# Performance work log

Measured on AMD Instinct MI355X. Metric: run time of the kernel, lower is better.

Reference implementation:

```python
import jax, jax.numpy as jnp
import numpy as np

B, N, DIM, NL, E = 8, 4096, 128, 3, 524288
NN = B * N


def setup_inputs() -> dict:
    key = jax.random.key(0)
    kx, ke, kw = jax.random.split(key, 3)
    x = jax.random.normal(kx, (B, N, DIM), dtype=jnp.float32)
    batch_edge_index = jax.random.randint(ke, (2, E), 0, NN, dtype=jnp.int32)
    wks = jax.random.split(kw, NL)
    Ws = jnp.stack([jax.random.normal(k, (DIM, DIM), dtype=jnp.float32) / np.sqrt(DIM)
                    for k in wks])  # [NL, DIM, DIM]
    bs = jnp.zeros((NL, DIM), dtype=jnp.float32)
    return {"x": x, "batch_edge_index": batch_edge_index, "Ws": Ws, "bs": bs}


def _gcn_layer(x, W, b, row, col, deg_inv_sqrt, n):
    # PyG GCNConv: h = x @ W; symmetric normalization over edges+self-loops;
    # scatter-add messages at targets (col); add bias.
    h = x @ W  # [n, DIM]
    norm = deg_inv_sqrt[row] * deg_inv_sqrt[col]  # [E+n]
    msg = h[row] * norm[:, None]  # gather at sources, scale
    return jax.ops.segment_sum(msg, col, num_segments=n) + b


def reference(x, batch_edge_index, Ws, bs):
    nb, npts, d = x.shape
    n = nb * npts
    h = x.reshape(n, d)
    # add self-loops once (same edge structure for all layers)
    loops = jnp.arange(n, dtype=batch_edge_index.dtype)
    row = jnp.concatenate([batch_edge_index[0], loops])
    col = jnp.concatenate([batch_edge_index[1], loops])
    deg = jax.ops.segment_sum(jnp.ones_like(col, dtype=h.dtype), col, num_segments=n)
    deg_inv_sqrt = jnp.where(deg > 0, jax.lax.rsqrt(jnp.maximum(deg, 1e-12)), 0.0)
    for i in range(NL):
        out = _gcn_layer(h, Ws[i], bs[i], row, col, deg_inv_sqrt, n)
        h = jax.nn.relu(h + out)  # residual + relu (dropout = identity in eval)
    return h.reshape(nb, npts, d)
```

## Files before the change

### kernel.cpp

```cpp
#include <hip/hip_runtime.h>


typedef __attribute__((ext_vector_type(8))) short short8;
typedef __attribute__((ext_vector_type(4))) float f32x4;
typedef __attribute__((ext_vector_type(2))) float f32x2;
typedef __attribute__((ext_vector_type(2))) unsigned u32x2;

__device__ inline ushort f2bf(float f) {
    union { float f; unsigned u; } v; v.f = f;
    unsigned u = v.u;
    return (ushort)((u + 0x7fffu + ((u >> 16) & 1u)) >> 16);
}
__device__ inline float2 bf2f(unsigned u) {
    union { unsigned i; float f; } a, b;
    a.i = u << 16;
    b.i = u & 0xffff0000u;
    return make_float2(a.f, b.f);
}
__device__ inline f32x4 bf4(u32x2 v) {
    float2 a = bf2f(v.x), b = bf2f(v.y);
    f32x4 r = { a.x, a.y, b.x, b.y };
    return r;
}
__device__ inline short8 pack8(f32x4 a, f32x4 b) {
    short8 r = { (short)f2bf(a.x), (short)f2bf(a.y), (short)f2bf(a.z), (short)f2bf(a.w),
                 (short)f2bf(b.x), (short)f2bf(b.y), (short)f2bf(b.z), (short)f2bf(b.w) };
    return r;
}
__device__ inline unsigned char f2fp8(float f) {
    return (unsigned char)(__builtin_amdgcn_cvt_pk_fp8_f32(f, f, 0, false) & 0xff);
}
__device__ inline unsigned pack4fp8(f32x4 v) {
    unsigned u = (unsigned)__builtin_amdgcn_cvt_pk_fp8_f32(v.x, v.y, 0, false);
    u = (unsigned)__builtin_amdgcn_cvt_pk_fp8_f32(v.z, v.w, (int)u, true);
    return u;
}
__device__ inline f32x4 fp8x4(unsigned v) {
    f32x2 lo = __builtin_amdgcn_cvt_pk_f32_fp8((int)v, false);
    f32x2 hi = __builtin_amdgcn_cvt_pk_f32_fp8((int)v, true);
    f32x4 r = { lo.x, lo.y, hi.x, hi.y };
    return r;
}

__global__ __launch_bounds__(256) void k_scan1(const int* __restrict__ deg,
                                               int* __restrict__ offs,
                                               int* __restrict__ bsum, int n) {
    __shared__ int sm[256];
    int t = threadIdx.x, i = blockIdx.x * 256 + t;
    int v = (i < n) ? deg[i] : 0;
    sm[t] = v;
    __syncthreads();
    for (int off = 1; off < 256; off <<= 1) {
        int u = (t >= off) ? sm[t - off] : 0;
        __syncthreads();
        sm[t] += u;
        __syncthreads();
    }
    if (i < n) offs[i] = sm[t] - v;
    if (t == 255) bsum[blockIdx.x] = sm[255];
}

__global__ __launch_bounds__(256) void k_scan3(int* __restrict__ offs,
                                               const int* __restrict__ bsum,
                                               const int* __restrict__ deg,
                                               int* __restrict__ cnt,
                                               float* __restrict__ dis,
                                               unsigned* __restrict__ g32,
                                               int n, int E) {
    __shared__ int red[256];
    int t = threadIdx.x, bid = blockIdx.x;
    red[t] = (t < 128 && t < bid) ? bsum[t] : 0;
    __syncthreads();
    for (int off = 128; off >= 1; off >>= 1) {
        if (t < off) red[t] += red[t + off];
        __syncthreads();
    }
    int base = red[0];
    int i = bid * 256 + t;
    float dv = 0.f;
    if (i < n) {
        int o = offs[i] + base;
        offs[i] = o;
        cnt[i] = o;
        dv = rsqrtf((float)(deg[i] + 1));
        dis[i] = dv;
    }
    if (i == 0) offs[n] = E;
    if (i < 32) g32[(size_t)n * 32 + i] = 0;

    int lane = t & 63;
    int wbase = bid * 256 + (t & ~63);
    int hl = lane & 31, sel = lane >> 5;
    for (int rr = 0; rr < 64; rr += 2) {
        int row = wbase + rr + sel;
        float d = __shfl(dv, rr + sel, 64);
        if (row < n) {
            unsigned u = g32[(size_t)row * 32 + hl];
            g32[(size_t)row * 32 + hl] = pack4fp8(fp8x4(u) * d);
        }
    }
}

__global__ void k_csr(const int* __restrict__ row, const int* __restrict__ col,
                      int* __restrict__ cnt, ushort* __restrict__ csru, int E) {
    int i = blockIdx.x * blockDim.x + threadIdx.x;
    if (i < E) {
        int c = col[i];
        int p = atomicAdd(&cnt[c], 1);
        csru[p] = (ushort)row[i];
    }
}

#define GEMM_MAIN(A0, A1, A2, A3)                                               \
    f32x4 acc[8] = {};                                                          \
    _Pragma("unroll")                                                           \
    for (int nf = 0; nf < 8; ++nf) {                                            \
        const unsigned* wr = &Wl[nf * 16 + c][0];                               \
        int sx = (c & 7) << 2;                                                  \
        int b = q * 4;                                                          \
        short8 b0 = *(const short8*)(wr + ((b +  0) ^ sx));                     \
        short8 b1 = *(const short8*)(wr + ((b + 16) ^ sx));                     \
        short8 b2 = *(const short8*)(wr + ((b + 32) ^ sx));                     \
        short8 b3 = *(const short8*)(wr + ((b + 48) ^ sx));                     \
        acc[nf] = __builtin_amdgcn_mfma_f32_16x16x32_bf16(A0, b0, acc[nf], 0, 0, 0); \
        acc[nf] = __builtin_amdgcn_mfma_f32_16x16x32_bf16(A1, b1, acc[nf], 0, 0, 0); \
        acc[nf] = __builtin_amdgcn_mfma_f32_16x16x32_bf16(A2, b2, acc[nf], 0, 0, 0); \
        acc[nf] = __builtin_amdgcn_mfma_f32_16x16x32_bf16(A3, b3, acc[nf], 0, 0, 0); \
    }

#define GEMM_STORE(D0, D1, D2, D3)                                              \
    _Pragma("unroll")                                                           \
    for (int nf = 0; nf < 8; ++nf) {                                            \
        int gc = nf * 16 + c;                                                   \
        g[(size_t)(rb + q * 4 + 0) * 128 + gc] = f2fp8(acc[nf][0] * (D0));      \
        g[(size_t)(rb + q * 4 + 1) * 128 + gc] = f2fp8(acc[nf][1] * (D1));      \
        g[(size_t)(rb + q * 4 + 2) * 128 + gc] = f2fp8(acc[nf][2] * (D2));      \
        g[(size_t)(rb + q * 4 + 3) * 128 + gc] = f2fp8(acc[nf][3] * (D3));      \
    }

#define W_STAGE(TILE)                                                            \
    __shared__ unsigned Wl[128][64];                                             \
    int tid = threadIdx.x;                                                       \
    {                                                                            \
        int nn = tid & 127, hf = tid >> 7;                                       \
        for (int qq = 0; qq < 32; ++qq) {                                        \
            int k2 = hf * 32 + qq;                                               \
            float lo = W[(size_t)(2 * k2) * 128 + nn];                           \
            float hi = W[(size_t)(2 * k2 + 1) * 128 + nn];                       \
            Wl[nn][k2 ^ ((nn & 7) << 2)] = ((unsigned)f2bf(hi) << 16) | f2bf(lo);\
        }                                                                        \
    }                                                                            \
    __syncthreads();                                                             \
    int w = tid >> 6, l = tid & 63;                                              \
    int rb = (TILE) * 64 + w * 16;                                               \
    int c = l & 15, q = l >> 4;

__global__ __launch_bounds__(256) void k_gemm(const unsigned* __restrict__ hb,
                                              const float* __restrict__ W,
                                              const float* __restrict__ dis,
                                              unsigned char* __restrict__ g, int n) {
    W_STAGE(blockIdx.x)
    const short8* arow = (const short8*)(hb + (size_t)(rb + c) * 64);
    short8 a0 = arow[q], a1 = arow[4 + q], a2 = arow[8 + q], a3 = arow[12 + q];
    GEMM_MAIN(a0, a1, a2, a3)
    float d0 = dis[rb + q * 4 + 0], d1 = dis[rb + q * 4 + 1];
    float d2 = dis[rb + q * 4 + 2], d3 = dis[rb + q * 4 + 3];
    GEMM_STORE(d0, d1, d2, d3)
}

__global__ __launch_bounds__(256) void k_l0(const float* __restrict__ x,
                                            const float* __restrict__ W,
                                            unsigned char* __restrict__ g,
                                            const int* __restrict__ col,
                                            int* __restrict__ deg,
                                            int n, int E) {
    int gtiles = n >> 6;
    if ((int)blockIdx.x >= gtiles) {
        int i = ((int)blockIdx.x - gtiles) * 256 + threadIdx.x;
        if (i < E) atomicAdd(&deg[col[i]], 1);
        return;
    }
    W_STAGE((int)blockIdx.x)
    const f32x4* xr = (const f32x4*)(x + (size_t)(rb + c) * 128);
    short8 a0 = pack8(xr[q * 2 +  0], xr[q * 2 +  1]);
    short8 a1 = pack8(xr[q * 2 +  8], xr[q * 2 +  9]);
    short8 a2 = pack8(xr[q * 2 + 16], xr[q * 2 + 17]);
    short8 a3 = pack8(xr[q * 2 + 24], xr[q * 2 + 25]);
    GEMM_MAIN(a0, a1, a2, a3)
    GEMM_STORE(1.f, 1.f, 1.f, 1.f)
}

__global__ __launch_bounds__(256) void k_gather(const unsigned* __restrict__ g32,
                                                unsigned* __restrict__ hb,
                                                const float* __restrict__ dis,
                                                const float* __restrict__ bias,
                                                const int* __restrict__ offs,
                                                const ushort* __restrict__ csru,
                                                const float* __restrict__ xres,
                                                float* __restrict__ outp,
                                                int n, int use_x, int last) {
    int wid = threadIdx.x >> 6, lane = threadIdx.x & 63;
    int sel = lane >> 5, hl = lane & 31;
    int node = blockIdx.x * 8 + wid * 2 + sel;
    if (node >= n) return;

    f32x4 acc = fp8x4(g32[(size_t)node * 32 + hl]);
    int s = offs[node];
    int deg = offs[node + 1] - s;
    for (int j0 = 0; j0 < deg; j0 += 32) {
        int rem = deg - j0;
        int m = rem < 32 ? rem : 32;
        int idx = (hl < m) ? (int)__builtin_nontemporal_load(&csru[s + j0 + hl]) : n;
        int mc = (m + 15) & ~15;
        for (int t = 0; t < mc; t += 16) {
            unsigned v[16];
#pragma unroll
            for (int u = 0; u < 16; ++u) {
                int r = __shfl(idx, t + u, 32);
                v[u] = g32[(size_t)r * 32 + hl];
            }
            f32x4 s0 = (fp8x4(v[0]) + fp8x4(v[1])) + (fp8x4(v[2]) + fp8x4(v[3]));
            f32x4 s1 = (fp8x4(v[4]) + fp8x4(v[5])) + (fp8x4(v[6]) + fp8x4(v[7]));
            f32x4 s2 = (fp8x4(v[8]) + fp8x4(v[9])) + (fp8x4(v[10]) + fp8x4(v[11]));
            f32x4 s3 = (fp8x4(v[12]) + fp8x4(v[13])) + (fp8x4(v[14]) + fp8x4(v[15]));
            acc += (s0 + s1) + (s2 + s3);
        }
    }
    float dn = dis[node];
    f32x4 bv = ((const f32x4*)bias)[hl];
    f32x4 hv;
    if (use_x) {
        hv = __builtin_nontemporal_load(&((const f32x4*)xres)[(size_t)node * 32 + hl]);
    } else {
        u32x2 h2 = __builtin_nontemporal_load(&((const u32x2*)hb)[(size_t)node * 32 + hl]);
        hv = bf4(h2);
    }
    f32x4 o = acc * dn + hv + bv;
    o.x = fmaxf(o.x, 0.f); o.y = fmaxf(o.y, 0.f);
    o.z = fmaxf(o.z, 0.f); o.w = fmaxf(o.w, 0.f);
    if (last) {
        __builtin_nontemporal_store(o, &((f32x4*)outp)[(size_t)node * 32 + hl]);
    } else {
        u32x2 pk;
        pk.x = ((unsigned)f2bf(o.y) << 16) | f2bf(o.x);
        pk.y = ((unsigned)f2bf(o.w) << 16) | f2bf(o.z);
        __builtin_nontemporal_store(pk, &((u32x2*)hb)[(size_t)node * 32 + hl]);
    }
}

static inline size_t al256(size_t x) { return (x + 255) & ~(size_t)255; }

extern "C" void kernel_launch(void* const* d_in, const int* in_sizes, int n_in,
                              void* d_out, int out_size, void* d_ws, size_t ws_size,
                              hipStream_t stream) {
    const float* x  = (const float*)d_in[0];
    const int*   ei = (const int*)d_in[1];
    const float* Ws = (const float*)d_in[2];
    const float* bs = (const float*)d_in[3];
    int n  = in_sizes[0] / 128;
    int E  = in_sizes[1] / 2;
    int NL = in_sizes[2] / (128 * 128);
    const int* rowp = ei;
    const int* colp = ei + E;

    char* ws = (char*)d_ws;
    size_t gplane  = al256((size_t)(n + 1) * 128);
    size_t hplane  = al256((size_t)(n + 1) * 256);
    unsigned char* g  = (unsigned char*)ws;
    unsigned*      hb = (unsigned*)(ws + gplane);
    char* p = ws + gplane + hplane;
    float* dis  = (float*)p;               p += al256((size_t)n * 4);
    int*   deg  = (int*)p;                 p += al256((size_t)n * 4);
    int*   offs = (int*)p;                 p += al256((size_t)(n + 1) * 4);
    int*   cnt  = (int*)p;                 p += al256((size_t)n * 4);
    int*   bsum = (int*)p;                 p += 512;
    ushort* csru = (ushort*)p;

    int nb = (n + 255) / 256;
    int gtiles = n / 64;
    int eblocks = (E + 255) / 256;

    (void)hipMemsetAsync(deg, 0, (size_t)n * 4, stream);
    k_l0<<<gtiles + eblocks, 256, 0, stream>>>(x, Ws, g, colp, deg, n, E);
    k_scan1<<<nb, 256, 0, stream>>>(deg, offs, bsum, n);
    k_scan3<<<nb, 256, 0, stream>>>(offs, bsum, deg, cnt, dis, (unsigned*)g, n, E);
    k_csr<<<eblocks, 256, 0, stream>>>(rowp, colp, cnt, csru, E);

    for (int l = 0; l < NL; ++l) {
        int last = (l + 1 == NL);
        if (l > 0)
            k_gemm<<<gtiles, 256, 0, stream>>>(hb, Ws + (size_t)l * 128 * 128,
                                               dis, g, n);
        k_gather<<<(n + 7) / 8, 256, 0, stream>>>((const unsigned*)g, hb, dis,
                                                  bs + (size_t)l * 128,
                                                  offs, csru, x,
                                                  (float*)d_out, n,
                                                  l == 0, last);
    }
}
```

Measured before the change: 142.3 us.

## Overlap layer-0 GEMM with CSR fill and fold degree scaling into GEMM store

```diff
diff --git a/kernel.cpp b/kernel.cpp
--- a/kernel.cpp
+++ b/kernel.cpp
@@ -30,16 +30,16 @@
 __device__ inline unsigned char f2fp8(float f) {
     return (unsigned char)(__builtin_amdgcn_cvt_pk_fp8_f32(f, f, 0, false) & 0xff);
 }
-__device__ inline unsigned pack4fp8(f32x4 v) {
-    unsigned u = (unsigned)__builtin_amdgcn_cvt_pk_fp8_f32(v.x, v.y, 0, false);
-    u = (unsigned)__builtin_amdgcn_cvt_pk_fp8_f32(v.z, v.w, (int)u, true);
-    return u;
-}
 __device__ inline f32x4 fp8x4(unsigned v) {
     f32x2 lo = __builtin_amdgcn_cvt_pk_f32_fp8((int)v, false);
     f32x2 hi = __builtin_amdgcn_cvt_pk_f32_fp8((int)v, true);
     f32x4 r = { lo.x, lo.y, hi.x, hi.y };
     return r;
+}
+
+__global__ void k_deg(const int* __restrict__ col, int* __restrict__ deg, int E) {
+    int i = blockIdx.x * blockDim.x + threadIdx.x;
+    if (i < E) atomicAdd(&deg[col[i]], 1);
 }
 
 __global__ __launch_bounds__(256) void k_scan1(const int* __restrict__ deg,
@@ -77,38 +77,14 @@
     }
     int base = red[0];
     int i = bid * 256 + t;
-    float dv = 0.f;
     if (i < n) {
         int o = offs[i] + base;
         offs[i] = o;
         cnt[i] = o;
-        dv = rsqrtf((float)(deg[i] + 1));
-        dis[i] = dv;
+        dis[i] = rsqrtf((float)(deg[i] + 1));
     }
     if (i == 0) offs[n] = E;
     if (i < 32) g32[(size_t)n * 32 + i] = 0;
-
-    int lane = t & 63;
-    int wbase = bid * 256 + (t & ~63);
-    int hl = lane & 31, sel = lane >> 5;
-    for (int rr = 0; rr < 64; rr += 2) {
-        int row = wbase + rr + sel;
-        float d = __shfl(dv, rr + sel, 64);
-        if (row < n) {
-            unsigned u = g32[(size_t)row * 32 + hl];
-            g32[(size_t)row * 32 + hl] = pack4fp8(fp8x4(u) * d);
-        }
-    }
-}
-
-__global__ void k_csr(const int* __restrict__ row, const int* __restrict__ col,
-                      int* __restrict__ cnt, ushort* __restrict__ csru, int E) {
-    int i = blockIdx.x * blockDim.x + threadIdx.x;
-    if (i < E) {
-        int c = col[i];
-        int p = atomicAdd(&cnt[c], 1);
-        csru[p] = (ushort)row[i];
-    }
 }
 
 #define GEMM_MAIN(A0, A1, A2, A3)                                               \
@@ -161,23 +137,33 @@
                                               unsigned char* __restrict__ g, int n) {
     W_STAGE(blockIdx.x)
     const short8* arow = (const short8*)(hb + (size_t)(rb + c) * 64);
-    short8 a0 = arow[q], a1 = arow[4 + q], a2 = arow[8 + q], a3 = arow[12 + q];
+    short8 a0 = __builtin_nontemporal_load(&arow[q]);
+    short8 a1 = __builtin_nontemporal_load(&arow[4 + q]);
+    short8 a2 = __builtin_nontemporal_load(&arow[8 + q]);
+    short8 a3 = __builtin_nontemporal_load(&arow[12 + q]);
     GEMM_MAIN(a0, a1, a2, a3)
     float d0 = dis[rb + q * 4 + 0], d1 = dis[rb + q * 4 + 1];
     float d2 = dis[rb + q * 4 + 2], d3 = dis[rb + q * 4 + 3];
     GEMM_STORE(d0, d1, d2, d3)
 }
 
-__global__ __launch_bounds__(256) void k_l0(const float* __restrict__ x,
-                                            const float* __restrict__ W,
-                                            unsigned char* __restrict__ g,
-                                            const int* __restrict__ col,
-                                            int* __restrict__ deg,
-                                            int n, int E) {
+__global__ __launch_bounds__(256) void k_l0b(const float* __restrict__ x,
+                                             const float* __restrict__ W,
+                                             const float* __restrict__ dis,
+                                             unsigned char* __restrict__ g,
+                                             const int* __restrict__ rowp,
+                                             const int* __restrict__ colp,
+                                             int* __restrict__ cnt,
+                                             ushort* __restrict__ csru,
+                                             int n, int E) {
     int gtiles = n >> 6;
     if ((int)blockIdx.x >= gtiles) {
         int i = ((int)blockIdx.x - gtiles) * 256 + threadIdx.x;
-        if (i < E) atomicAdd(&deg[col[i]], 1);
+        if (i < E) {
+            int cc = colp[i];
+            int p = atomicAdd(&cnt[cc], 1);
+            csru[p] = (ushort)rowp[i];
+        }
         return;
     }
     W_STAGE((int)blockIdx.x)
@@ -187,7 +173,9 @@
     short8 a2 = pack8(xr[q * 2 + 16], xr[q * 2 + 17]);
     short8 a3 = pack8(xr[q * 2 + 24], xr[q * 2 + 25]);
     GEMM_MAIN(a0, a1, a2, a3)
-    GEMM_STORE(1.f, 1.f, 1.f, 1.f)
+    float d0 = dis[rb + q * 4 + 0], d1 = dis[rb + q * 4 + 1];
+    float d2 = dis[rb + q * 4 + 2], d3 = dis[rb + q * 4 + 3];
+    GEMM_STORE(d0, d1, d2, d3)
 }
 
 __global__ __launch_bounds__(256) void k_gather(const unsigned* __restrict__ g32,
@@ -204,28 +192,6 @@
     int node = blockIdx.x * 8 + wid * 2 + sel;
     if (node >= n) return;
 
-    f32x4 acc = fp8x4(g32[(size_t)node * 32 + hl]);
-    int s = offs[node];
-    int deg = offs[node + 1] - s;
-    for (int j0 = 0; j0 < deg; j0 += 32) {
-        int rem = deg - j0;
-        int m = rem < 32 ? rem : 32;
-        int idx = (hl < m) ? (int)__builtin_nontemporal_load(&csru[s + j0 + hl]) : n;
-        int mc = (m + 15) & ~15;
-        for (int t = 0; t < mc; t += 16) {
-            unsigned v[16];
-#pragma unroll
-            for (int u = 0; u < 16; ++u) {
-                int r = __shfl(idx, t + u, 32);
-                v[u] = g32[(size_t)r * 32 + hl];
-            }
-            f32x4 s0 = (fp8x4(v[0]) + fp8x4(v[1])) + (fp8x4(v[2]) + fp8x4(v[3]));
-            f32x4 s1 = (fp8x4(v[4]) + fp8x4(v[5])) + (fp8x4(v[6]) + fp8x4(v[7]));
-            f32x4 s2 = (fp8x4(v[8]) + fp8x4(v[9])) + (fp8x4(v[10]) + fp8x4(v[11]));
-            f32x4 s3 = (fp8x4(v[12]) + fp8x4(v[13])) + (fp8x4(v[14]) + fp8x4(v[15]));
-            acc += (s0 + s1) + (s2 + s3);
-        }
-    }
     float dn = dis[node];
     f32x4 bv = ((const f32x4*)bias)[hl];
     f32x4 hv;
@@ -235,6 +201,38 @@
         u32x2 h2 = __builtin_nontemporal_load(&((const u32x2*)hb)[(size_t)node * 32 + hl]);
         hv = bf4(h2);
     }
+
+    f32x4 acc = fp8x4(g32[(size_t)node * 32 + hl]);
+    int s = offs[node];
+    int deg = offs[node + 1] - s;
+    for (int j0 = 0; j0 < deg; j0 += 32) {
+        int rem = deg - j0;
+        int m = rem < 32 ? rem : 32;
+        int idx = (hl < m) ? (int)__builtin_nontemporal_load(&csru[s + j0 + hl]) : n;
+        int mc = (m + 7) & ~7;
+        unsigned v[32];
+#pragma unroll
+        for (int b = 0; b < 4; ++b) {
+            if (b * 8 < mc) {
+#pragma unroll
+                for (int u = 0; u < 8; ++u) {
+                    int r = __shfl(idx, b * 8 + u, 32);
+                    v[b * 8 + u] = g32[(size_t)r * 32 + hl];
+                }
+            }
+        }
+#pragma unroll
+        for (int b = 0; b < 4; ++b) {
+            if (b * 8 < mc) {
+                f32x4 s0 = (fp8x4(v[b * 8 + 0]) + fp8x4(v[b * 8 + 1])) +
+                           (fp8x4(v[b * 8 + 2]) + fp8x4(v[b * 8 + 3]));
+                f32x4 s1 = (fp8x4(v[b * 8 + 4]) + fp8x4(v[b * 8 + 5])) +
+                           (fp8x4(v[b * 8 + 6]) + fp8x4(v[b * 8 + 7]));
+                acc += s0 + s1;
+            }
+        }
+    }
+
     f32x4 o = acc * dn + hv + bv;
     o.x = fmaxf(o.x, 0.f); o.y = fmaxf(o.y, 0.f);
     o.z = fmaxf(o.z, 0.f); o.w = fmaxf(o.w, 0.f);
@@ -281,10 +279,11 @@
     int eblocks = (E + 255) / 256;
 
     (void)hipMemsetAsync(deg, 0, (size_t)n * 4, stream);
-    k_l0<<<gtiles + eblocks, 256, 0, stream>>>(x, Ws, g, colp, deg, n, E);
+    k_deg<<<eblocks, 256, 0, stream>>>(colp, deg, E);
     k_scan1<<<nb, 256, 0, stream>>>(deg, offs, bsum, n);
     k_scan3<<<nb, 256, 0, stream>>>(offs, bsum, deg, cnt, dis, (unsigned*)g, n, E);
-    k_csr<<<eblocks, 256, 0, stream>>>(rowp, colp, cnt, csru, E);
+    k_l0b<<<gtiles + eblocks, 256, 0, stream>>>(x, Ws, dis, g, rowp, colp,
+                                                cnt, csru, n, E);
 
     for (int l = 0; l < NL; ++l) {
         int last = (l + 1 == NL);
```

Result: faster. 136.8 us (-3.8%).
